# Kernel optimization log

Hardware: AMD Instinct MI355X
Metric: run time of the kernel (lower is better)

Reference implementation:

```python
import jax, jax.numpy as jnp
import numpy as np

K = 15.0          # sigmoid sharpness in get_approxi
THETA2 = 400.0    # gaussian 'theta2' parameter
LOSS_WEIGHT = 1.0


def obb2poly_le90(boxes):
    # boxes [..., 5] = (x, y, w, h, a) -> poly [..., 8]
    x, y, w, h, a = (boxes[..., i] for i in range(5))
    cosa, sina = jnp.cos(a), jnp.sin(a)
    wx, wy = 0.5 * w * cosa, 0.5 * w * sina
    hx, hy = -0.5 * h * sina, 0.5 * h * cosa
    return jnp.stack([
        x - wx - hx, y - wy - hy,
        x + wx - hx, y + wy - hy,
        x + wx + hx, y + wy + hy,
        x - wx + hx, y - wy + hy,
    ], axis=-1)


def setup_inputs() -> dict:
    key = jax.random.key(0)
    k1, k2, k3, k4, k5, k6 = jax.random.split(key, 6)
    N, M = 256, 512

    def make_boxes(k):
        u = jax.random.uniform(k, (N, 5), dtype=jnp.float32)
        cx = 100.0 + 300.0 * u[:, 0]
        cy = 100.0 + 300.0 * u[:, 1]
        w = 20.0 + 100.0 * u[:, 2]
        h = 20.0 + 100.0 * u[:, 3]
        a = (u[:, 4] - 0.5) * (jnp.pi / 2)
        return jnp.stack([cx, cy, w, h, a], axis=-1)

    pred = make_boxes(k1)
    target = make_boxes(k2)
    mask = 512.0 * jax.random.uniform(k3, (N, M, 2), dtype=jnp.float32)
    grad_x = jax.random.normal(k4, (N, M), dtype=jnp.float32)
    grad_y = jax.random.normal(k5, (N, M), dtype=jnp.float32)
    offset = 50.0 * jax.random.uniform(k6, (N, 2), dtype=jnp.float32)
    return {"pred": pred, "target": target, "mask": mask,
            "grad_x": grad_x, "grad_y": grad_y, "offset": offset}


def _my_loss(pred, target, mask, grad_x, grad_y, offset):
    # pred/target [N,5], mask [N,M,2], grad_x/grad_y [N,M], offset [N,2]
    px = pred[:, 0] - offset[:, 0]   # [N]
    py = pred[:, 1] - offset[:, 1]
    pw, ph, pa = pred[:, 2], pred[:, 3], pred[:, 4]
    gx = target[:, 0] - offset[:, 0]
    gy = target[:, 1] - offset[:, 1]
    gw, gh, ga = target[:, 2], target[:, 3], target[:, 4]

    mx, my = mask[..., 0], mask[..., 1]            # [N,M]
    dx = mx - gx[:, None]
    dy = my - gy[:, None]
    d = jnp.sqrt(dx * dx + dy * dy)                # [N,M]
    acos_arg = jnp.clip((gx[:, None] - mx) / d, -1.0, 1.0)
    acosv = jnp.arccos(acos_arg)
    beta = jnp.where(gy[:, None] >= my, ga[:, None] + acosv, ga[:, None] - acosv)

    d_w = jnp.abs(d * jnp.cos(beta))
    d_h = jnp.abs(d * jnp.sin(beta))
    sig = jax.nn.sigmoid
    approxi_1 = (1.0 - sig(K * (d_w - gw[:, None]) / gw[:, None])) * \
                (1.0 - sig(K * (d_h - gh[:, None]) / gh[:, None]))  # [N,M]

    d_w_p = pw[:, None] * d_w / gw[:, None]
    d_h_p = ph[:, None] * d_h / gh[:, None]
    zeros = jnp.zeros_like(d_w_p)
    boxes = jnp.stack([zeros, zeros, 2.0 * d_w_p, 2.0 * d_h_p,
                       jnp.broadcast_to(pa[:, None], d_w_p.shape)], axis=-1)
    pts = obb2poly_le90(boxes)                     # [N,M,8]

    half_pi = jnp.pi / 2
    q2 = (beta > -half_pi) & (beta <= 0.0)
    q3 = (beta > -jnp.pi) & (beta <= -half_pi)
    q4 = (beta > half_pi) & (beta <= jnp.pi)
    # default (q1: 0 < beta <= pi/2) -> corner 0
    gpx = jnp.where(q2, pts[..., 2], jnp.where(q3, pts[..., 4], jnp.where(q4, pts[..., 6], pts[..., 0])))
    gpy = jnp.where(q2, pts[..., 3], jnp.where(q3, pts[..., 5], jnp.where(q4, pts[..., 7], pts[..., 1])))
    guass_x = px[:, None] + gpx                    # [N,M]
    guass_y = py[:, None] + gpy

    # approxi_2[n,i,j] = exp(+||guass_i - mask_j||^2 / (2*theta2^2)) / (2*pi*theta2)
    dgx = guass_x[:, :, None] - mx[:, None, :]
    dgy = guass_y[:, :, None] - my[:, None, :]
    approxi_2 = jnp.exp((dgx * dgx + dgy * dgy) / (2.0 * THETA2 * THETA2)) / (2.0 * jnp.pi * THETA2)

    # w[n,i,j] = gx_i*gx_j + gy_i*gy_j
    w = grad_x[:, :, None] * grad_x[:, None, :] + grad_y[:, :, None] * grad_y[:, None, :]

    loss_per_box = jnp.mean(w * approxi_2 * approxi_1[:, None, :], axis=(1, 2))  # [N]
    return loss_per_box


def reference(pred, target, mask, grad_x, grad_y, offset):
    loss_per_box = _my_loss(pred, target, mask, grad_x, grad_y, offset)
    return LOSS_WEIGHT * jnp.mean(loss_per_box)  # reduction='mean'
```

## Files before the change

kernel.cpp:

```cpp
#include <hip/hip_runtime.h>
#include <math.h>

typedef float v2f __attribute__((ext_vector_type(2)));

#define N_BOX   256
#define M_PTS   512
#define S_SPLIT 8
#define BLK     256
#define M2_PER  (M_PTS / S_SPLIT)
#define GRID    (N_BOX * S_SPLIT)
#define LEAF_BLKS 64
#define N_LEAF    (GRID / LEAF_BLKS)

__global__ __launch_bounds__(BLK, 8) void loss_onepass(
    const float* __restrict__ pred,
    const float* __restrict__ target,
    const float* __restrict__ mask,
    const float* __restrict__ gradx,
    const float* __restrict__ grady,
    const float* __restrict__ offset,
    float* __restrict__ ws,
    float* __restrict__ out)
{
    __shared__ float4 sP[M2_PER];
    __shared__ float  sW[4];
    __shared__ int    sLast;

    const int bid = blockIdx.x;
    const int n = bid >> 3;
    const int s = bid & 7;
    const int t = threadIdx.x;

    const float offx = offset[n * 2 + 0];
    const float offy = offset[n * 2 + 1];
    const float px = pred[n * 5 + 0] - offx;
    const float py = pred[n * 5 + 1] - offy;
    const float pw = pred[n * 5 + 2];
    const float ph = pred[n * 5 + 3];
    const float pa = pred[n * 5 + 4];
    const float gx = target[n * 5 + 0] - offx;
    const float gy = target[n * 5 + 1] - offy;
    const float gw = target[n * 5 + 2];
    const float gh = target[n * 5 + 3];
    const float ga = target[n * 5 + 4];

    float sinpa, cospa, singa, cosga;
    sincosf(pa, &sinpa, &cospa);
    sincosf(ga, &singa, &cosga);

    const float THETA2   = 400.0f;
    const float LOG2E    = 1.4426950408889634f;
    const float c1       = LOG2E / (2.0f * THETA2 * THETA2);
    const float rs       = sqrtf(c1);
    const float inv_norm = 1.0f / (2.0f * (float)M_PI * THETA2);

    const float pwg = pw / gw, phg = ph / gh;
    const float cwx = pwg * cospa, swx = pwg * sinpa;
    const float chx = phg * cospa, shx = phg * sinpa;
    const float absinga = fabsf(singa);
    const float kA  = 15.0f * LOG2E / gw;
    const float kH  = 15.0f * LOG2E / gh;
    const float kB  = 15.0f * LOG2E;
    const float pxrs = px * rs, pyrs = py * rs;
    const bool  gaPos = (ga > 0.0f), gaNeg = (ga < 0.0f);

    const float2* mask2 = (const float2*)mask;
    const size_t  base  = (size_t)n * M_PTS;

    if (t < M2_PER) {
        const int m = s * M2_PER + t;
        const float2 mp = mask2[base + m];
        const float dx = mp.x - gx;
        const float dy = mp.y - gy;
        const float u = singa * dy - cosga * dx;
        const float v = -(cosga * dy + singa * dx);
        const float au = fabsf(u), av = fabsf(v);
        const float eA = __builtin_amdgcn_exp2f(fmaf(au, kA, -kB));
        const float eB = __builtin_amdgcn_exp2f(fmaf(av, kH, -kB));
        const float B  = inv_norm / ((1.0f + eA) * (1.0f + eB));
        sP[t] = make_float4(mp.x * rs, mp.y * rs,
                            gradx[base + m] * B, grady[base + m] * B);
    }

    v2f Gx, Gy, gvx, gvy;
#pragma unroll
    for (int r = 0; r < 2; ++r) {
        const int m = t + (r << 8);
        const float2 mp = mask2[base + m];
        const float dx = mp.x - gx;
        const float dy = mp.y - gy;
        const float u = singa * dy - cosga * dx;
        const float v = -(cosga * dy + singa * dx);
        const bool sgaOk = gaPos ? (dy <= 0.0f) : (gaNeg ? (dy > 0.0f) : false);
        const bool wrap  = sgaOk && (dx > 0.0f) && (dx * absinga > fabsf(dy) * cosga);
        const float au = fabsf(u), av = fabsf(v);
        const float dws = (wrap || v > 0.0f) ? -au : au;
        const float dhs = (wrap || u > 0.0f) ? -av : av;
        const float gpx = dws * cwx - dhs * shx;
        const float gpy = dws * swx + dhs * chx;
        Gx[r]  = fmaf(gpx, rs, pxrs);
        Gy[r]  = fmaf(gpy, rs, pyrs);
        gvx[r] = gradx[base + m];
        gvy[r] = grady[base + m];
    }
    __syncthreads();

    v2f accz = (v2f)0.0f, accw = (v2f)0.0f;
#pragma unroll 4
    for (int m2 = 0; m2 < M2_PER; ++m2) {
        const float4 p = sP[m2];
        v2f dgx = Gx - p.x;
        v2f dgy = Gy - p.y;
        v2f sa  = dgx * dgx + dgy * dgy;
        v2f e;
        e.x = __builtin_amdgcn_exp2f(sa.x);
        e.y = __builtin_amdgcn_exp2f(sa.y);
        accz += e * p.z;
        accw += e * p.w;
    }

    v2f tot = accz * gvx + accw * gvy;
    float acc = tot.x + tot.y;
#pragma unroll
    for (int off = 32; off > 0; off >>= 1)
        acc += __shfl_down(acc, off, 64);
    if ((t & 63) == 0) sW[t >> 6] = acc;
    __syncthreads();

    float* part = ws;
    unsigned int* ctrL = (unsigned int*)ws + 4096;
    unsigned int* ctrM = (unsigned int*)ws + 5120;
    if (t == 0) {
        const float blockSum = sW[0] + sW[1] + sW[2] + sW[3];
        __hip_atomic_store(&part[bid], blockSum,
                           __ATOMIC_RELAXED, __HIP_MEMORY_SCOPE_AGENT);
        asm volatile("s_waitcnt vmcnt(0)" ::: "memory");
        int last = 0;
        const int g = bid >> 6;
        unsigned int* slot = ctrL + g * 32;
        const unsigned int pL = slot[4];
        const unsigned int oL = __hip_atomic_fetch_add(slot, 1u,
                                    __ATOMIC_RELAXED, __HIP_MEMORY_SCOPE_AGENT);
        if (((oL - pL) & (LEAF_BLKS - 1)) == (LEAF_BLKS - 1)) {
            const unsigned int pM = ctrM[4];
            const unsigned int oM = __hip_atomic_fetch_add(ctrM, 1u,
                                        __ATOMIC_RELAXED, __HIP_MEMORY_SCOPE_AGENT);
            if (((oM - pM) & (N_LEAF - 1)) == (N_LEAF - 1)) last = 1;
        }
        sLast = last;
    }
    __syncthreads();

    if (sLast) {
        float a2 = 0.0f;
#pragma unroll
        for (int i = 0; i < 8; ++i)
            a2 += __hip_atomic_load(&part[t + (i << 8)],
                      __ATOMIC_RELAXED, __HIP_MEMORY_SCOPE_AGENT);
#pragma unroll
        for (int off = 32; off > 0; off >>= 1)
            a2 += __shfl_down(a2, off, 64);
        if ((t & 63) == 0) sW[t >> 6] = a2;
        __syncthreads();
        if (t == 0) {
            const float scale = 1.0f / ((float)N_BOX * (float)M_PTS * (float)M_PTS);
            out[0] = (sW[0] + sW[1] + sW[2] + sW[3]) * scale;
        }
    }
}

extern "C" void kernel_launch(void* const* d_in, const int* in_sizes, int n_in,
                              void* d_out, int out_size, void* d_ws, size_t ws_size,
                              hipStream_t stream) {
    const float* pred   = (const float*)d_in[0];
    const float* target = (const float*)d_in[1];
    const float* mask   = (const float*)d_in[2];
    const float* gradx  = (const float*)d_in[3];
    const float* grady  = (const float*)d_in[4];
    const float* offset = (const float*)d_in[5];
    float* out = (float*)d_out;
    float* ws  = (float*)d_ws;

    hipLaunchKernelGGL(loss_onepass, dim3(GRID), dim3(BLK), 0, stream,
                       pred, target, mask, gradx, grady, offset, ws, out);
}
```

Measured before the change: 84.67 us.

## Split into precompute kernel and expand squared distance to cut inner-loop ops

Moves the per-point geometry (G coordinates, sigmoid weights) into a separate precompute kernel that writes float4 arrays to workspace, so each of the eight split blocks per box no longer recomputes all 512 G points. The pair loop expands |G-m|^2 as |G|^2 - 2G·m + |m|^2 and folds exp2(|m|^2) into the per-point weight, giving two FMAs per exponent instead of subtract/multiply/add. This adds a second launch and a global round trip. Splitting the exponential can also overflow or lose precision when the |m|^2 term is large.

```diff
diff --git a/kernel.cpp b/kernel.cpp
--- a/kernel.cpp
+++ b/kernel.cpp
@@ -12,24 +12,19 @@
 #define LEAF_BLKS 64
 #define N_LEAF    (GRID / LEAF_BLKS)
 
-__global__ __launch_bounds__(BLK, 8) void loss_onepass(
+
+__global__ __launch_bounds__(512) void precompute(
     const float* __restrict__ pred,
     const float* __restrict__ target,
     const float* __restrict__ mask,
     const float* __restrict__ gradx,
     const float* __restrict__ grady,
     const float* __restrict__ offset,
-    float* __restrict__ ws,
-    float* __restrict__ out)
+    float4* __restrict__ P1,
+    float4* __restrict__ P2)
 {
-    __shared__ float4 sP[M2_PER];
-    __shared__ float  sW[4];
-    __shared__ int    sLast;
-
-    const int bid = blockIdx.x;
-    const int n = bid >> 3;
-    const int s = bid & 7;
-    const int t = threadIdx.x;
+    const int n = blockIdx.x;
+    const int m = threadIdx.x;
 
     const float offx = offset[n * 2 + 0];
     const float offy = offset[n * 2 + 1];
@@ -65,60 +60,80 @@
     const bool  gaPos = (ga > 0.0f), gaNeg = (ga < 0.0f);
 
     const float2* mask2 = (const float2*)mask;
-    const size_t  base  = (size_t)n * M_PTS;
-
-    if (t < M2_PER) {
-        const int m = s * M2_PER + t;
-        const float2 mp = mask2[base + m];
-        const float dx = mp.x - gx;
-        const float dy = mp.y - gy;
-        const float u = singa * dy - cosga * dx;
-        const float v = -(cosga * dy + singa * dx);
-        const float au = fabsf(u), av = fabsf(v);
-        const float eA = __builtin_amdgcn_exp2f(fmaf(au, kA, -kB));
-        const float eB = __builtin_amdgcn_exp2f(fmaf(av, kH, -kB));
-        const float B  = inv_norm / ((1.0f + eA) * (1.0f + eB));
-        sP[t] = make_float4(mp.x * rs, mp.y * rs,
-                            gradx[base + m] * B, grady[base + m] * B);
-    }
-
-    v2f Gx, Gy, gvx, gvy;
-#pragma unroll
-    for (int r = 0; r < 2; ++r) {
-        const int m = t + (r << 8);
-        const float2 mp = mask2[base + m];
-        const float dx = mp.x - gx;
-        const float dy = mp.y - gy;
-        const float u = singa * dy - cosga * dx;
-        const float v = -(cosga * dy + singa * dx);
-        const bool sgaOk = gaPos ? (dy <= 0.0f) : (gaNeg ? (dy > 0.0f) : false);
-        const bool wrap  = sgaOk && (dx > 0.0f) && (dx * absinga > fabsf(dy) * cosga);
-        const float au = fabsf(u), av = fabsf(v);
-        const float dws = (wrap || v > 0.0f) ? -au : au;
-        const float dhs = (wrap || u > 0.0f) ? -av : av;
-        const float gpx = dws * cwx - dhs * shx;
-        const float gpy = dws * swx + dhs * chx;
-        Gx[r]  = fmaf(gpx, rs, pxrs);
-        Gy[r]  = fmaf(gpy, rs, pyrs);
-        gvx[r] = gradx[base + m];
-        gvy[r] = grady[base + m];
-    }
+    const size_t  idx   = (size_t)n * M_PTS + m;
+
+    const float2 mp = mask2[idx];
+    const float dx = mp.x - gx;
+    const float dy = mp.y - gy;
+    const float u = singa * dy - cosga * dx;
+    const float v = -(cosga * dy + singa * dx);
+    const bool sgaOk = gaPos ? (dy <= 0.0f) : (gaNeg ? (dy > 0.0f) : false);
+    const bool wrap  = sgaOk && (dx > 0.0f) && (dx * absinga > fabsf(dy) * cosga);
+    const float au = fabsf(u), av = fabsf(v);
+    const float dws = (wrap || v > 0.0f) ? -au : au;
+    const float dhs = (wrap || u > 0.0f) ? -av : av;
+    const float gpx = dws * cwx - dhs * shx;
+    const float gpy = dws * swx + dhs * chx;
+    const float gvx = gradx[idx];
+    const float gvy = grady[idx];
+
+    const float eA = __builtin_amdgcn_exp2f(fmaf(au, kA, -kB));
+    const float eB = __builtin_amdgcn_exp2f(fmaf(av, kH, -kB));
+    const float B  = inv_norm / ((1.0f + eA) * (1.0f + eB));
+
+    const float Gx = fmaf(gpx, rs, pxrs);
+    const float Gy = fmaf(gpy, rs, pyrs);
+    P1[idx] = make_float4(Gx, Gy, gvx, gvy);
+
+    const float mxrs = mp.x * rs, myrs = mp.y * rs;
+    const float C   = mxrs * mxrs + myrs * myrs;
+    const float e2C = __builtin_amdgcn_exp2f(C);
+    P2[idx] = make_float4(-2.0f * mxrs, -2.0f * myrs,
+                          gvx * B * e2C, gvy * B * e2C);
+}
+
+__global__ __launch_bounds__(BLK, 8) void pair_protocol(
+    const float4* __restrict__ P1,
+    const float4* __restrict__ P2,
+    float* __restrict__ ws,
+    float* __restrict__ out)
+{
+    __shared__ float4 sP[M2_PER];
+    __shared__ float  sW[4];
+    __shared__ int    sLast;
+
+    const int bid = blockIdx.x;
+    const int n = bid >> 3;
+    const int s = bid & 7;
+    const int t = threadIdx.x;
+
+    const size_t base = (size_t)n * M_PTS;
+    if (t < M2_PER) sP[t] = P2[base + s * M2_PER + t];
+
+    const float4 g0 = P1[base + t];
+    const float4 g1 = P1[base + t + 256];
     __syncthreads();
+
+    v2f Gx = {g0.x, g1.x};
+    v2f Gy = {g0.y, g1.y};
+    v2f Rx = Gx * Gx + Gy * Gy;
 
     v2f accz = (v2f)0.0f, accw = (v2f)0.0f;
 #pragma unroll 4
     for (int m2 = 0; m2 < M2_PER; ++m2) {
         const float4 p = sP[m2];
-        v2f dgx = Gx - p.x;
-        v2f dgy = Gy - p.y;
-        v2f sa  = dgx * dgx + dgy * dgy;
+        v2f tE;
+        tE.x = fmaf(p.x, Gx.x, fmaf(p.y, Gy.x, Rx.x));
+        tE.y = fmaf(p.x, Gx.y, fmaf(p.y, Gy.y, Rx.y));
         v2f e;
-        e.x = __builtin_amdgcn_exp2f(sa.x);
-        e.y = __builtin_amdgcn_exp2f(sa.y);
+        e.x = __builtin_amdgcn_exp2f(tE.x);
+        e.y = __builtin_amdgcn_exp2f(tE.y);
         accz += e * p.z;
         accw += e * p.w;
     }
 
+    v2f gvx = {g0.z, g1.z};
+    v2f gvy = {g0.w, g1.w};
     v2f tot = accz * gvx + accw * gvy;
     float acc = tot.x + tot.y;
 #pragma unroll
@@ -181,6 +196,11 @@
     float* out = (float*)d_out;
     float* ws  = (float*)d_ws;
 
-    hipLaunchKernelGGL(loss_onepass, dim3(GRID), dim3(BLK), 0, stream,
-                       pred, target, mask, gradx, grady, offset, ws, out);
+    float4* P1 = (float4*)((char*)d_ws + (1u << 20));
+    float4* P2 = (float4*)((char*)d_ws + (4u << 20));
+
+    hipLaunchKernelGGL(precompute, dim3(N_BOX), dim3(M_PTS), 0, stream,
+                       pred, target, mask, gradx, grady, offset, P1, P2);
+    hipLaunchKernelGGL(pair_protocol, dim3(GRID), dim3(BLK), 0, stream,
+                       P1, P2, ws, out);
 }
```

Measured after the change: 87.10 us. +2.9%, slower.
